# Optimization experiments

Hardware: AMD Instinct MI355X
Metric: run time of the kernel (lower is better)

Reference implementation:

```python
import jax, jax.numpy as jnp
import numpy as np

BIG = 1e9
EPS_BETA = 1e-6
EPS_BN = 1e-5

N_NODES = 50000
N_EDGES = 800000
IN_DIM = 128
OUT_DIM = 128


def setup_inputs() -> dict:
    key = jax.random.key(0)
    ks = jax.random.split(key, 8)
    h = jax.random.normal(ks[0], (N_NODES, IN_DIM), dtype=jnp.float32)
    src = jax.random.randint(ks[1], (N_EDGES,), 0, N_NODES, dtype=jnp.int32)
    dst = jax.random.randint(ks[2], (N_EDGES,), 0, N_NODES, dtype=jnp.int32)
    sigma_GD = jax.random.uniform(ks[3], (N_EDGES,), dtype=jnp.float32)
    fc_w = jax.random.normal(ks[4], (IN_DIM, OUT_DIM), dtype=jnp.float32) / np.sqrt(IN_DIM)
    fc_b = jax.random.normal(ks[5], (OUT_DIM,), dtype=jnp.float32) * 0.01
    attn_w = jax.random.normal(ks[6], (2 * OUT_DIM, 1), dtype=jnp.float32) / np.sqrt(2 * OUT_DIM)
    attn_b = jax.random.normal(ks[7], (1,), dtype=jnp.float32) * 0.01
    bn_gamma = jnp.ones((OUT_DIM,), dtype=jnp.float32)
    bn_beta = jnp.zeros((OUT_DIM,), dtype=jnp.float32)
    return {"h": h, "src": src, "dst": dst, "sigma_GD": sigma_GD,
            "fc_w": fc_w, "fc_b": fc_b, "attn_w": attn_w, "attn_b": attn_b,
            "bn_gamma": bn_gamma, "bn_beta": bn_beta}


def reference(h, src, dst, sigma_GD, fc_w, fc_b, attn_w, attn_b, bn_gamma, bn_beta):
    n = h.shape[0]
    # node projection
    z = h @ fc_w + fc_b                                   # [N, D]
    z = jnp.where(jnp.isinf(z), BIG, z)
    # per-edge attention logits: concat(src,dst) @ W == src@W1 + dst@W2 (avoid concat materialization)
    d = z.shape[1]
    w_src, w_dst = attn_w[:d], attn_w[d:]
    z_src = z[src]                                        # [E, D]
    a = z_src @ w_src + z[dst] @ w_dst + attn_b           # [E, 1]
    a = jnp.where(jnp.isinf(a), BIG, a)
    e = jax.nn.leaky_relu(a, negative_slope=0.01)[:, 0]   # [E]
    # segment softmax over incoming edges (mailbox softmax)
    m = jax.ops.segment_max(e, dst, num_segments=n)       # [N]
    ex = jnp.exp(e - m[dst])
    denom = jax.ops.segment_sum(ex, dst, num_segments=n)  # [N]
    alpha = ex / denom[dst]                               # [E]
    # beta: sigma_GD normalized per destination node
    bsum = jax.ops.segment_sum(sigma_GD, dst, num_segments=n)
    beta = sigma_GD / (bsum[dst] + EPS_BETA)              # [E]
    # weighted scatter-sum of source features
    h_new = jax.ops.segment_sum((alpha * beta)[:, None] * z_src, dst, num_segments=n)  # [N, D]
    h_new = jnp.where(jnp.isinf(h_new), BIG, h_new)
    # BatchNorm1d (training-mode batch stats, biased variance, as torch does)
    mu = h_new.mean(axis=0)
    var = ((h_new - mu) ** 2).mean(axis=0)
    h_bn = (h_new - mu) * jax.lax.rsqrt(var + EPS_BN) * bn_gamma + bn_beta
    return jax.nn.elu(h_bn)
```

## Files before the change

kernel.cpp:

```cpp
#include <hip/hip_runtime.h>
#include <hip/hip_fp16.h>
#include <math.h>

#define N_NODES 50000
#define N_EDGES 800000
#define BIGV 1000000000.0f
#define NBLK_SCAN 196
#define NBLK_GEMM 3125

typedef _Float16 half8 __attribute__((ext_vector_type(8)));
typedef float floatx4 __attribute__((ext_vector_type(4)));

__device__ __forceinline__ float clampinf(float x) { return isinf(x) ? BIGV : x; }

__global__ __launch_bounds__(256) void k_wcast(const float* __restrict__ W,
                                               __half* __restrict__ wt,
                                               int* __restrict__ cursor,
                                               float* __restrict__ bns)
{
    int idx = blockIdx.x * 256 + threadIdx.x;
    int n = idx >> 7, k = idx & 127;
    wt[idx] = __float2half(W[k * 128 + n]);
    for (int i = idx; i < N_NODES; i += 16384) cursor[i] = 0;
    if (idx < 256) bns[idx] = 0.f;
}

__global__ __launch_bounds__(256) void k_gemm(
    const float* __restrict__ h, const __half* __restrict__ wt,
    const float* __restrict__ bias, const float* __restrict__ attn_w,
    const int* __restrict__ dst, __half* __restrict__ zh,
    float* __restrict__ sv, float* __restrict__ tv,
    int* __restrict__ cursor, int* __restrict__ rank)
{
    __shared__ _Float16 hA[16][136];
    __shared__ float spart[4][16], tpart[4][16];

    const int tid = threadIdx.x;
    const int lane = tid & 63;
    const int wv = tid >> 6;
    const int l16 = lane & 15;
    const int oct = lane >> 4;
    const int n0 = wv << 5;
    const int node0 = blockIdx.x << 4;

    const int e = blockIdx.x * 256 + tid;
    const int d = dst[e];
    {
        const float4* h4 = (const float4*)(h + (size_t)node0 * 128);
        for (int i = tid; i < 512; i += 256) {
            int r = i >> 5, c4 = i & 31;
            float4 v = h4[i];
            union { __half2 h2[2]; uint2 u; } pk;
            pk.h2[0] = __floats2half2_rn(v.x, v.y);
            pk.h2[1] = __floats2half2_rn(v.z, v.w);
            *(uint2*)&hA[r][c4 << 2] = pk.u;
        }
    }
    rank[e] = atomicAdd(&cursor[d], 1);

    half8 bfrag[4][2];
    #pragma unroll
    for (int kk = 0; kk < 4; ++kk)
        #pragma unroll
        for (int t = 0; t < 2; ++t)
            bfrag[kk][t] = *(const half8*)(wt + (size_t)(n0 + t * 16 + l16) * 128
                                              + kk * 32 + oct * 8);

    const float bv0 = bias[n0 + l16],         bv1 = bias[n0 + 16 + l16];
    const float ws0 = attn_w[n0 + l16],       ws1 = attn_w[n0 + 16 + l16];
    const float wd0 = attn_w[128 + n0 + l16], wd1 = attn_w[128 + n0 + 16 + l16];

    __syncthreads();

    floatx4 acc0 = {0.f, 0.f, 0.f, 0.f};
    floatx4 acc1 = {0.f, 0.f, 0.f, 0.f};
    #pragma unroll
    for (int kk = 0; kk < 4; ++kk) {
        half8 a = *(const half8*)&hA[l16][(kk << 5) + (oct << 3)];
        acc0 = __builtin_amdgcn_mfma_f32_16x16x32_f16(a, bfrag[kk][0], acc0, 0, 0, 0);
        acc1 = __builtin_amdgcn_mfma_f32_16x16x32_f16(a, bfrag[kk][1], acc1, 0, 0, 0);
    }

    float s_acc[4], t_acc[4];
    #pragma unroll
    for (int r = 0; r < 4; ++r) {
        float z0 = clampinf(acc0[r] + bv0);
        float z1 = clampinf(acc1[r] + bv1);
        const int row = (oct << 2) + r;
        zh[(size_t)(node0 + row) * 128 + n0 + l16]      = __float2half(z0);
        zh[(size_t)(node0 + row) * 128 + n0 + 16 + l16] = __float2half(z1);
        s_acc[r] = z0 * ws0 + z1 * ws1;
        t_acc[r] = z0 * wd0 + z1 * wd1;
    }
    #pragma unroll
    for (int r = 0; r < 4; ++r) {
        #pragma unroll
        for (int o = 1; o < 16; o <<= 1) {
            s_acc[r] += __shfl_xor(s_acc[r], o);
            t_acc[r] += __shfl_xor(t_acc[r], o);
        }
    }
    if (l16 == 0) {
        #pragma unroll
        for (int r = 0; r < 4; ++r) {
            spart[wv][(oct << 2) + r] = s_acc[r];
            tpart[wv][(oct << 2) + r] = t_acc[r];
        }
    }
    __syncthreads();
    if (tid < 16) {
        sv[node0 + tid] = spart[0][tid] + spart[1][tid] + spart[2][tid] + spart[3][tid];
        tv[node0 + tid] = tpart[0][tid] + tpart[1][tid] + tpart[2][tid] + tpart[3][tid];
    }
}

__global__ __launch_bounds__(256) void k_scan_bsum(const int* __restrict__ cursor,
                                                   int* __restrict__ bsum)
{
    __shared__ int s[256];
    const int t = threadIdx.x;
    const int idx = blockIdx.x * 256 + t;
    s[t] = (idx < N_NODES) ? cursor[idx] : 0;
    __syncthreads();
    for (int off = 128; off; off >>= 1) {
        if (t < off) s[t] += s[t + off];
        __syncthreads();
    }
    if (t == 0) bsum[blockIdx.x] = s[0];
}

__global__ __launch_bounds__(256) void k_scan_final(const int* __restrict__ bsum,
                                                    const int* __restrict__ cursor_in,
                                                    int* __restrict__ colptr)
{
    __shared__ int rs[256];
    __shared__ int s[256];
    const int t = threadIdx.x;

    int rv = (t < NBLK_SCAN) ? bsum[t] : 0;
    rs[t] = rv;
    __syncthreads();
    for (int off = 1; off < 256; off <<= 1) {
        int u = (t >= off) ? rs[t - off] : 0;
        __syncthreads();
        rs[t] += u;
        __syncthreads();
    }
    const int broot = (blockIdx.x > 0) ? rs[blockIdx.x - 1] : 0;
    if (blockIdx.x == 0 && t == 255) colptr[N_NODES] = rs[255];

    const int idx = blockIdx.x * 256 + t;
    int v = (idx < N_NODES) ? cursor_in[idx] : 0;
    s[t] = v;
    __syncthreads();
    for (int off = 1; off < 256; off <<= 1) {
        int u = (t >= off) ? s[t - off] : 0;
        __syncthreads();
        s[t] += u;
        __syncthreads();
    }
    if (idx < N_NODES) colptr[idx] = broot + s[t] - v;
}

__global__ void k_scatter(const int* __restrict__ src, const int* __restrict__ dst,
                          const float* __restrict__ sigma,
                          const int* __restrict__ rank, const int* __restrict__ colptr,
                          const float* __restrict__ sv, const float* __restrict__ tv,
                          const float* __restrict__ attn_b,
                          float4* __restrict__ recs)
{
    int e = blockIdx.x * 256 + threadIdx.x;
    if (e < N_EDGES) {
        int s = src[e];
        int d = dst[e];
        float a = sv[s] + tv[d] + attn_b[0];
        a = clampinf(a);
        float ev = a > 0.f ? a : 0.01f * a;
        int pos = colptr[d] + rank[e];
        float4 rec;
        rec.x = __int_as_float(s);
        rec.y = sigma[e];
        rec.z = ev;
        rec.w = 0.f;
        recs[pos] = rec;
    }
}

__global__ __launch_bounds__(256) void k_agg(
    const int* __restrict__ colptr, const float4* __restrict__ recs,
    const __half* __restrict__ zh, float* __restrict__ out)
{
    const int lane = threadIdx.x & 63;
    const int node = blockIdx.x * 4 + (threadIdx.x >> 6);
    if (node >= N_NODES) return;
    const int base = colptr[node];
    const int deg = colptr[node + 1] - base;

    const int grp = lane >> 4;
    const int l16 = lane & 15;
    float acc[8] = {0.f, 0.f, 0.f, 0.f, 0.f, 0.f, 0.f, 0.f};

    if (deg > 0) {
        if (deg <= 64) {
            int sidx = 0; float sig = 0.f, e = -INFINITY;
            if (lane < deg) {
                float4 r = recs[base + lane];
                sidx = __float_as_int(r.x); sig = r.y; e = r.z;
            }
            float m = e;
            for (int o = 32; o; o >>= 1) m = fmaxf(m, __shfl_xor(m, o));
            float p = (lane < deg) ? __expf(e - m) : 0.f;
            float dn = p, bs = sig;
            for (int o = 32; o; o >>= 1) {
                dn += __shfl_xor(dn, o);
                bs += __shfl_xor(bs, o);
            }
            const float coef = p * sig * (1.0f / dn) / (bs + 1e-6f);
            for (int c = 0; c < deg; c += 4) {
                const int j = c + grp;
                const int js = (j < deg) ? j : 0;
                float cf = __shfl(coef, js);
                int sj = __shfl(sidx, js);
                if (j < deg) {
                    uint4 raw = *(const uint4*)(zh + ((size_t)sj << 7) + (l16 << 3));
                    const __half2* hp = (const __half2*)&raw;
                    #pragma unroll
                    for (int k = 0; k < 4; ++k) {
                        float2 f = __half22float2(hp[k]);
                        acc[2*k]   = fmaf(cf, f.x, acc[2*k]);
                        acc[2*k+1] = fmaf(cf, f.y, acc[2*k+1]);
                    }
                }
            }
        } else {
            float m = -INFINITY;
            for (int i = lane; i < deg; i += 64) m = fmaxf(m, recs[base + i].z);
            for (int o = 32; o; o >>= 1) m = fmaxf(m, __shfl_xor(m, o));
            float dn = 0.f, bs = 0.f;
            for (int i = lane; i < deg; i += 64) {
                float4 r = recs[base + i];
                dn += __expf(r.z - m); bs += r.y;
            }
            for (int o = 32; o; o >>= 1) {
                dn += __shfl_xor(dn, o);
                bs += __shfl_xor(bs, o);
            }
            const float scale = (1.0f / dn) / (bs + 1e-6f);
            for (int c = 0; c < deg; c += 64) {
                int i = c + lane;
                int sidx = 0; float coef = 0.f;
                if (i < deg) {
                    float4 r = recs[base + i];
                    sidx = __float_as_int(r.x);
                    coef = __expf(r.z - m) * r.y * scale;
                }
                const int cnt = min(64, deg - c);
                for (int j = 0; j < cnt; j += 4) {
                    const int jj = j + grp;
                    const int js = (jj < cnt) ? jj : 0;
                    float cf = __shfl(coef, js);
                    int sj = __shfl(sidx, js);
                    if (jj < cnt) {
                        uint4 raw = *(const uint4*)(zh + ((size_t)sj << 7) + (l16 << 3));
                        const __half2* hp = (const __half2*)&raw;
                        #pragma unroll
                        for (int k = 0; k < 4; ++k) {
                            float2 f = __half22float2(hp[k]);
                            acc[2*k]   = fmaf(cf, f.x, acc[2*k]);
                            acc[2*k+1] = fmaf(cf, f.y, acc[2*k+1]);
                        }
                    }
                }
            }
        }
    }
    #pragma unroll
    for (int k = 0; k < 8; ++k) {
        acc[k] += __shfl_xor(acc[k], 16);
        acc[k] += __shfl_xor(acc[k], 32);
    }
    if (grp == 0) {
        float4 o0, o1;
        o0.x = clampinf(acc[0]); o0.y = clampinf(acc[1]);
        o0.z = clampinf(acc[2]); o0.w = clampinf(acc[3]);
        o1.x = clampinf(acc[4]); o1.y = clampinf(acc[5]);
        o1.z = clampinf(acc[6]); o1.w = clampinf(acc[7]);
        float4* op = (float4*)(out + (size_t)node * 128 + (l16 << 3));
        op[0] = o0; op[1] = o1;
    }
}

__global__ __launch_bounds__(256) void k_bnstats(const float* __restrict__ hnew,
                                                 float* __restrict__ sums)
{
    const int f = threadIdx.x & 127;
    const int half_ = threadIdx.x >> 7;
    float s = 0.f, q = 0.f;
    for (int node = blockIdx.x * 2 + half_; node < N_NODES; node += gridDim.x * 2) {
        float v = hnew[(size_t)node * 128 + f];
        s += v;
        q += v * v;
    }
    __shared__ float ls[256], lq[256];
    ls[threadIdx.x] = s; lq[threadIdx.x] = q;
    __syncthreads();
    if (half_ == 0) {
        s += ls[threadIdx.x + 128];
        q += lq[threadIdx.x + 128];
        atomicAdd(&sums[f], s);
        atomicAdd(&sums[128 + f], q);
    }
}

__global__ __launch_bounds__(256) void k_bnapply(float* __restrict__ io,
                                                 const float* __restrict__ sums,
                                                 const float* __restrict__ gamma,
                                                 const float* __restrict__ beta)
{
    const size_t idx = (size_t)blockIdx.x * 256 + threadIdx.x;
    const int f = (int)(idx & 127);
    const float invn = 1.0f / (float)N_NODES;
    float mu = sums[f] * invn;
    float var = fmaxf(sums[128 + f] * invn - mu * mu, 0.f);
    float rs = rsqrtf(var + 1e-5f);
    float x = io[idx];
    float y = (x - mu) * rs * gamma[f] + beta[f];
    io[idx] = y > 0.f ? y : expm1f(y);
}

extern "C" void kernel_launch(void* const* d_in, const int* in_sizes, int n_in,
                              void* d_out, int out_size, void* d_ws, size_t ws_size,
                              hipStream_t stream)
{
    const float* h      = (const float*)d_in[0];
    const int*   src    = (const int*)  d_in[1];
    const int*   dst    = (const int*)  d_in[2];
    const float* sigma  = (const float*)d_in[3];
    const float* fc_w   = (const float*)d_in[4];
    const float* fc_b   = (const float*)d_in[5];
    const float* attn_w = (const float*)d_in[6];
    const float* attn_b = (const float*)d_in[7];
    const float* gamma  = (const float*)d_in[8];
    const float* beta   = (const float*)d_in[9];
    float* out = (float*)d_out;

    float4* recs   = (float4*)d_ws;
    __half* zh     = (__half*)(recs + N_EDGES);
    float*  sv     = (float*)(zh + (size_t)N_NODES * 128);
    float*  tv     = sv + N_NODES;
    float*  bns    = tv + N_NODES;
    int*    colptr = (int*)(bns + 256);
    int*    cursor = colptr + 50004;
    int*    bsum   = cursor + N_NODES;
    int*    broot  = bsum + 256;
    __half* wt     = (__half*)(broot + 256);
    int*    rank   = (int*)(wt + 128 * 128);

    k_wcast     <<<64, 256, 0, stream>>>(fc_w, wt, cursor, bns);
    k_gemm      <<<NBLK_GEMM, 256, 0, stream>>>(h, wt, fc_b, attn_w, dst,
                                                zh, sv, tv, cursor, rank);
    k_scan_bsum <<<NBLK_SCAN, 256, 0, stream>>>(cursor, bsum);
    k_scan_final<<<NBLK_SCAN, 256, 0, stream>>>(bsum, cursor, colptr);
    k_scatter   <<<N_EDGES / 256, 256, 0, stream>>>(src, dst, sigma, rank, colptr,
                                                    sv, tv, attn_b, recs);
    k_agg       <<<N_NODES / 4, 256, 0, stream>>>(colptr, recs, zh, out);
    k_bnstats   <<<256, 256, 0, stream>>>(out, bns);
    k_bnapply   <<<(N_NODES * 128) / 256, 256, 0, stream>>>(out, bns, gamma, beta);
}
```

Before: 230.8 us.

## Fuse all pipeline stages into one cooperative persistent kernel with grid syncs

Replaces the seven separate kernel launches (GEMM, two scan passes, scatter, aggregation, BN stats, BN apply) with a single cooperative persistent kernel that loops over work and uses grid-wide syncs between stages. The aim is to remove per-launch overhead and inter-kernel gaps. The BN apply step is also vectorised to float4. In exchange, the grid is capped by occupancy, so each stage gets fewer blocks, and each grid.sync adds its own cost; shared memory is reused through a union.

Result: slower. 883.2 us (+282.8%).

```diff
diff --git a/kernel.cpp b/kernel.cpp
--- a/kernel.cpp
+++ b/kernel.cpp
@@ -1,22 +1,31 @@
 #include <hip/hip_runtime.h>
+#include <hip/hip_cooperative_groups.h>
 #include <hip/hip_fp16.h>
 #include <math.h>
+
+namespace cg = cooperative_groups;
 
 #define N_NODES 50000
 #define N_EDGES 800000
 #define BIGV 1000000000.0f
 #define NBLK_SCAN 196
-#define NBLK_GEMM 3125
+#define N_TILES 3125
 
 typedef _Float16 half8 __attribute__((ext_vector_type(8)));
 typedef float floatx4 __attribute__((ext_vector_type(4)));
 
 __device__ __forceinline__ float clampinf(float x) { return isinf(x) ? BIGV : x; }
 
-__global__ __launch_bounds__(256) void k_wcast(const float* __restrict__ W,
-                                               __half* __restrict__ wt,
-                                               int* __restrict__ cursor,
-                                               float* __restrict__ bns)
+union SH {
+    struct { _Float16 hA[16][136]; float spart[4][16]; float tpart[4][16]; } g;
+    struct { int rs[256]; int s[256]; } sc;
+    struct { float ls[256]; float lq[256]; } bn;
+};
+
+__global__ __launch_bounds__(256) void k_pre(const float* __restrict__ W,
+                                             __half* __restrict__ wt,
+                                             int* __restrict__ cursor,
+                                             float* __restrict__ bns)
 {
     int idx = blockIdx.x * 256 + threadIdx.x;
     int n = idx >> 7, k = idx & 127;
@@ -25,152 +34,148 @@
     if (idx < 256) bns[idx] = 0.f;
 }
 
-__global__ __launch_bounds__(256) void k_gemm(
+__global__ __launch_bounds__(256) void k_mega(
     const float* __restrict__ h, const __half* __restrict__ wt,
     const float* __restrict__ bias, const float* __restrict__ attn_w,
-    const int* __restrict__ dst, __half* __restrict__ zh,
-    float* __restrict__ sv, float* __restrict__ tv,
-    int* __restrict__ cursor, int* __restrict__ rank)
+    const int* __restrict__ src, const int* __restrict__ dst,
+    const float* __restrict__ sigma, const float* __restrict__ attn_b,
+    __half* __restrict__ zh, float* __restrict__ sv, float* __restrict__ tv,
+    int* __restrict__ cursor, int* __restrict__ rank,
+    int* __restrict__ bsum, int* __restrict__ colptr,
+    float4* __restrict__ recs, float* __restrict__ out,
+    float* __restrict__ bns, const float* __restrict__ gamma,
+    const float* __restrict__ beta)
 {
-    __shared__ _Float16 hA[16][136];
-    __shared__ float spart[4][16], tpart[4][16];
+    __shared__ SH sh;
+    cg::grid_group grid = cg::this_grid();
 
     const int tid = threadIdx.x;
     const int lane = tid & 63;
     const int wv = tid >> 6;
     const int l16 = lane & 15;
     const int oct = lane >> 4;
-    const int n0 = wv << 5;
-    const int node0 = blockIdx.x << 4;
-
-    const int e = blockIdx.x * 256 + tid;
-    const int d = dst[e];
+
     {
-        const float4* h4 = (const float4*)(h + (size_t)node0 * 128);
-        for (int i = tid; i < 512; i += 256) {
-            int r = i >> 5, c4 = i & 31;
-            float4 v = h4[i];
-            union { __half2 h2[2]; uint2 u; } pk;
-            pk.h2[0] = __floats2half2_rn(v.x, v.y);
-            pk.h2[1] = __floats2half2_rn(v.z, v.w);
-            *(uint2*)&hA[r][c4 << 2] = pk.u;
-        }
-    }
-    rank[e] = atomicAdd(&cursor[d], 1);
-
-    half8 bfrag[4][2];
-    #pragma unroll
-    for (int kk = 0; kk < 4; ++kk)
+        const int n0 = wv << 5;
+        half8 bfrag[4][2];
         #pragma unroll
-        for (int t = 0; t < 2; ++t)
-            bfrag[kk][t] = *(const half8*)(wt + (size_t)(n0 + t * 16 + l16) * 128
-                                              + kk * 32 + oct * 8);
-
-    const float bv0 = bias[n0 + l16],         bv1 = bias[n0 + 16 + l16];
-    const float ws0 = attn_w[n0 + l16],       ws1 = attn_w[n0 + 16 + l16];
-    const float wd0 = attn_w[128 + n0 + l16], wd1 = attn_w[128 + n0 + 16 + l16];
-
-    __syncthreads();
-
-    floatx4 acc0 = {0.f, 0.f, 0.f, 0.f};
-    floatx4 acc1 = {0.f, 0.f, 0.f, 0.f};
-    #pragma unroll
-    for (int kk = 0; kk < 4; ++kk) {
-        half8 a = *(const half8*)&hA[l16][(kk << 5) + (oct << 3)];
-        acc0 = __builtin_amdgcn_mfma_f32_16x16x32_f16(a, bfrag[kk][0], acc0, 0, 0, 0);
-        acc1 = __builtin_amdgcn_mfma_f32_16x16x32_f16(a, bfrag[kk][1], acc1, 0, 0, 0);
-    }
-
-    float s_acc[4], t_acc[4];
-    #pragma unroll
-    for (int r = 0; r < 4; ++r) {
-        float z0 = clampinf(acc0[r] + bv0);
-        float z1 = clampinf(acc1[r] + bv1);
-        const int row = (oct << 2) + r;
-        zh[(size_t)(node0 + row) * 128 + n0 + l16]      = __float2half(z0);
-        zh[(size_t)(node0 + row) * 128 + n0 + 16 + l16] = __float2half(z1);
-        s_acc[r] = z0 * ws0 + z1 * ws1;
-        t_acc[r] = z0 * wd0 + z1 * wd1;
-    }
-    #pragma unroll
-    for (int r = 0; r < 4; ++r) {
-        #pragma unroll
-        for (int o = 1; o < 16; o <<= 1) {
-            s_acc[r] += __shfl_xor(s_acc[r], o);
-            t_acc[r] += __shfl_xor(t_acc[r], o);
-        }
-    }
-    if (l16 == 0) {
-        #pragma unroll
-        for (int r = 0; r < 4; ++r) {
-            spart[wv][(oct << 2) + r] = s_acc[r];
-            tpart[wv][(oct << 2) + r] = t_acc[r];
-        }
-    }
-    __syncthreads();
-    if (tid < 16) {
-        sv[node0 + tid] = spart[0][tid] + spart[1][tid] + spart[2][tid] + spart[3][tid];
-        tv[node0 + tid] = tpart[0][tid] + tpart[1][tid] + tpart[2][tid] + tpart[3][tid];
-    }
-}
-
-__global__ __launch_bounds__(256) void k_scan_bsum(const int* __restrict__ cursor,
-                                                   int* __restrict__ bsum)
-{
-    __shared__ int s[256];
-    const int t = threadIdx.x;
-    const int idx = blockIdx.x * 256 + t;
-    s[t] = (idx < N_NODES) ? cursor[idx] : 0;
-    __syncthreads();
-    for (int off = 128; off; off >>= 1) {
-        if (t < off) s[t] += s[t + off];
+        for (int kk = 0; kk < 4; ++kk)
+            #pragma unroll
+            for (int t = 0; t < 2; ++t)
+                bfrag[kk][t] = *(const half8*)(wt + (size_t)(n0 + t * 16 + l16) * 128
+                                                  + kk * 32 + oct * 8);
+        const float bv0 = bias[n0 + l16],         bv1 = bias[n0 + 16 + l16];
+        const float ws0 = attn_w[n0 + l16],       ws1 = attn_w[n0 + 16 + l16];
+        const float wd0 = attn_w[128 + n0 + l16], wd1 = attn_w[128 + n0 + 16 + l16];
+
+        for (int tile = blockIdx.x; tile < N_TILES; tile += gridDim.x) {
+            const int node0 = tile << 4;
+            const int e = tile * 256 + tid;
+            const int d = dst[e];
+            __syncthreads();
+            {
+                const float4* h4 = (const float4*)(h + (size_t)node0 * 128);
+                for (int i = tid; i < 512; i += 256) {
+                    int r = i >> 5, c4 = i & 31;
+                    float4 v = h4[i];
+                    union { __half2 h2[2]; uint2 u; } pk;
+                    pk.h2[0] = __floats2half2_rn(v.x, v.y);
+                    pk.h2[1] = __floats2half2_rn(v.z, v.w);
+                    *(uint2*)&sh.g.hA[r][c4 << 2] = pk.u;
+                }
+            }
+            rank[e] = atomicAdd(&cursor[d], 1);
+            __syncthreads();
+
+            floatx4 acc0 = {0.f, 0.f, 0.f, 0.f};
+            floatx4 acc1 = {0.f, 0.f, 0.f, 0.f};
+            #pragma unroll
+            for (int kk = 0; kk < 4; ++kk) {
+                half8 a = *(const half8*)&sh.g.hA[l16][(kk << 5) + (oct << 3)];
+                acc0 = __builtin_amdgcn_mfma_f32_16x16x32_f16(a, bfrag[kk][0], acc0, 0, 0, 0);
+                acc1 = __builtin_amdgcn_mfma_f32_16x16x32_f16(a, bfrag[kk][1], acc1, 0, 0, 0);
+            }
+
+            float s_acc[4], t_acc[4];
+            #pragma unroll
+            for (int r = 0; r < 4; ++r) {
+                float z0 = clampinf(acc0[r] + bv0);
+                float z1 = clampinf(acc1[r] + bv1);
+                const int row = (oct << 2) + r;
+                zh[(size_t)(node0 + row) * 128 + n0 + l16]      = __float2half(z0);
+                zh[(size_t)(node0 + row) * 128 + n0 + 16 + l16] = __float2half(z1);
+                s_acc[r] = z0 * ws0 + z1 * ws1;
+                t_acc[r] = z0 * wd0 + z1 * wd1;
+            }
+            #pragma unroll
+            for (int r = 0; r < 4; ++r) {
+                #pragma unroll
+                for (int o = 1; o < 16; o <<= 1) {
+                    s_acc[r] += __shfl_xor(s_acc[r], o);
+                    t_acc[r] += __shfl_xor(t_acc[r], o);
+                }
+            }
+            if (l16 == 0) {
+                #pragma unroll
+                for (int r = 0; r < 4; ++r) {
+                    sh.g.spart[wv][(oct << 2) + r] = s_acc[r];
+                    sh.g.tpart[wv][(oct << 2) + r] = t_acc[r];
+                }
+            }
+            __syncthreads();
+            if (tid < 16) {
+                sv[node0 + tid] = sh.g.spart[0][tid] + sh.g.spart[1][tid]
+                                + sh.g.spart[2][tid] + sh.g.spart[3][tid];
+                tv[node0 + tid] = sh.g.tpart[0][tid] + sh.g.tpart[1][tid]
+                                + sh.g.tpart[2][tid] + sh.g.tpart[3][tid];
+            }
+        }
+    }
+    __threadfence();
+    grid.sync();
+
+    if (blockIdx.x < NBLK_SCAN) {
+        const int idx = blockIdx.x * 256 + tid;
+        sh.sc.s[tid] = (idx < N_NODES) ? cursor[idx] : 0;
         __syncthreads();
-    }
-    if (t == 0) bsum[blockIdx.x] = s[0];
-}
-
-__global__ __launch_bounds__(256) void k_scan_final(const int* __restrict__ bsum,
-                                                    const int* __restrict__ cursor_in,
-                                                    int* __restrict__ colptr)
-{
-    __shared__ int rs[256];
-    __shared__ int s[256];
-    const int t = threadIdx.x;
-
-    int rv = (t < NBLK_SCAN) ? bsum[t] : 0;
-    rs[t] = rv;
-    __syncthreads();
-    for (int off = 1; off < 256; off <<= 1) {
-        int u = (t >= off) ? rs[t - off] : 0;
+        for (int off = 128; off; off >>= 1) {
+            if (tid < off) sh.sc.s[tid] += sh.sc.s[tid + off];
+            __syncthreads();
+        }
+        if (tid == 0) bsum[blockIdx.x] = sh.sc.s[0];
+    }
+    __threadfence();
+    grid.sync();
+
+    if (blockIdx.x < NBLK_SCAN) {
+        int rv = (tid < NBLK_SCAN) ? bsum[tid] : 0;
+        sh.sc.rs[tid] = rv;
         __syncthreads();
-        rs[t] += u;
+        for (int off = 1; off < 256; off <<= 1) {
+            int u = (tid >= off) ? sh.sc.rs[tid - off] : 0;
+            __syncthreads();
+            sh.sc.rs[tid] += u;
+            __syncthreads();
+        }
+        const int broot = (blockIdx.x > 0) ? sh.sc.rs[blockIdx.x - 1] : 0;
+        if (blockIdx.x == 0 && tid == 255) colptr[N_NODES] = sh.sc.rs[255];
+
+        const int idx = blockIdx.x * 256 + tid;
+        int v = (idx < N_NODES) ? cursor[idx] : 0;
+        sh.sc.s[tid] = v;
         __syncthreads();
-    }
-    const int broot = (blockIdx.x > 0) ? rs[blockIdx.x - 1] : 0;
-    if (blockIdx.x == 0 && t == 255) colptr[N_NODES] = rs[255];
-
-    const int idx = blockIdx.x * 256 + t;
-    int v = (idx < N_NODES) ? cursor_in[idx] : 0;
-    s[t] = v;
-    __syncthreads();
-    for (int off = 1; off < 256; off <<= 1) {
-        int u = (t >= off) ? s[t - off] : 0;
-        __syncthreads();
-        s[t] += u;
-        __syncthreads();
-    }
-    if (idx < N_NODES) colptr[idx] = broot + s[t] - v;
-}
-
-__global__ void k_scatter(const int* __restrict__ src, const int* __restrict__ dst,
-                          const float* __restrict__ sigma,
-                          const int* __restrict__ rank, const int* __restrict__ colptr,
-                          const float* __restrict__ sv, const float* __restrict__ tv,
-                          const float* __restrict__ attn_b,
-                          float4* __restrict__ recs)
-{
-    int e = blockIdx.x * 256 + threadIdx.x;
-    if (e < N_EDGES) {
+        for (int off = 1; off < 256; off <<= 1) {
+            int u = (tid >= off) ? sh.sc.s[tid - off] : 0;
+            __syncthreads();
+            sh.sc.s[tid] += u;
+            __syncthreads();
+        }
+        if (idx < N_NODES) colptr[idx] = broot + sh.sc.s[tid] - v;
+    }
+    __threadfence();
+    grid.sync();
+
+    for (int e = blockIdx.x * 256 + tid; e < N_EDGES; e += gridDim.x * 256) {
         int s = src[e];
         int d = dst[e];
         float a = sv[s] + tv[d] + attn_b[0];
@@ -184,83 +189,38 @@
         rec.w = 0.f;
         recs[pos] = rec;
     }
-}
-
-__global__ __launch_bounds__(256) void k_agg(
-    const int* __restrict__ colptr, const float4* __restrict__ recs,
-    const __half* __restrict__ zh, float* __restrict__ out)
-{
-    const int lane = threadIdx.x & 63;
-    const int node = blockIdx.x * 4 + (threadIdx.x >> 6);
-    if (node >= N_NODES) return;
-    const int base = colptr[node];
-    const int deg = colptr[node + 1] - base;
-
-    const int grp = lane >> 4;
-    const int l16 = lane & 15;
-    float acc[8] = {0.f, 0.f, 0.f, 0.f, 0.f, 0.f, 0.f, 0.f};
-
-    if (deg > 0) {
-        if (deg <= 64) {
-            int sidx = 0; float sig = 0.f, e = -INFINITY;
-            if (lane < deg) {
-                float4 r = recs[base + lane];
-                sidx = __float_as_int(r.x); sig = r.y; e = r.z;
-            }
-            float m = e;
-            for (int o = 32; o; o >>= 1) m = fmaxf(m, __shfl_xor(m, o));
-            float p = (lane < deg) ? __expf(e - m) : 0.f;
-            float dn = p, bs = sig;
-            for (int o = 32; o; o >>= 1) {
-                dn += __shfl_xor(dn, o);
-                bs += __shfl_xor(bs, o);
-            }
-            const float coef = p * sig * (1.0f / dn) / (bs + 1e-6f);
-            for (int c = 0; c < deg; c += 4) {
-                const int j = c + grp;
-                const int js = (j < deg) ? j : 0;
-                float cf = __shfl(coef, js);
-                int sj = __shfl(sidx, js);
-                if (j < deg) {
-                    uint4 raw = *(const uint4*)(zh + ((size_t)sj << 7) + (l16 << 3));
-                    const __half2* hp = (const __half2*)&raw;
-                    #pragma unroll
-                    for (int k = 0; k < 4; ++k) {
-                        float2 f = __half22float2(hp[k]);
-                        acc[2*k]   = fmaf(cf, f.x, acc[2*k]);
-                        acc[2*k+1] = fmaf(cf, f.y, acc[2*k+1]);
-                    }
-                }
-            }
-        } else {
-            float m = -INFINITY;
-            for (int i = lane; i < deg; i += 64) m = fmaxf(m, recs[base + i].z);
-            for (int o = 32; o; o >>= 1) m = fmaxf(m, __shfl_xor(m, o));
-            float dn = 0.f, bs = 0.f;
-            for (int i = lane; i < deg; i += 64) {
-                float4 r = recs[base + i];
-                dn += __expf(r.z - m); bs += r.y;
-            }
-            for (int o = 32; o; o >>= 1) {
-                dn += __shfl_xor(dn, o);
-                bs += __shfl_xor(bs, o);
-            }
-            const float scale = (1.0f / dn) / (bs + 1e-6f);
-            for (int c = 0; c < deg; c += 64) {
-                int i = c + lane;
-                int sidx = 0; float coef = 0.f;
-                if (i < deg) {
-                    float4 r = recs[base + i];
-                    sidx = __float_as_int(r.x);
-                    coef = __expf(r.z - m) * r.y * scale;
-                }
-                const int cnt = min(64, deg - c);
-                for (int j = 0; j < cnt; j += 4) {
-                    const int jj = j + grp;
-                    const int js = (jj < cnt) ? jj : 0;
+    __threadfence();
+    grid.sync();
+
+    for (int g4 = blockIdx.x; g4 < N_NODES / 4; g4 += gridDim.x) {
+        const int node = g4 * 4 + wv;
+        const int base = colptr[node];
+        const int deg = colptr[node + 1] - base;
+        const int grp = oct;
+        float acc[8] = {0.f, 0.f, 0.f, 0.f, 0.f, 0.f, 0.f, 0.f};
+
+        if (deg > 0) {
+            if (deg <= 64) {
+                int sidx = 0; float sig = 0.f, e = -INFINITY;
+                if (lane < deg) {
+                    float4 r = recs[base + lane];
+                    sidx = __float_as_int(r.x); sig = r.y; e = r.z;
+                }
+                float m = e;
+                for (int o = 32; o; o >>= 1) m = fmaxf(m, __shfl_xor(m, o));
+                float p = (lane < deg) ? __expf(e - m) : 0.f;
+                float dn = p, bs = sig;
+                for (int o = 32; o; o >>= 1) {
+                    dn += __shfl_xor(dn, o);
+                    bs += __shfl_xor(bs, o);
+                }
+                const float coef = p * sig * (1.0f / dn) / (bs + 1e-6f);
+                for (int c = 0; c < deg; c += 4) {
+                    const int j = c + grp;
+                    const int js = (j < deg) ? j : 0;
                     float cf = __shfl(coef, js);
                     int sj = __shfl(sidx, js);
-                    if (jj < cnt) {
+                    if (j < deg) {
                         uint4 raw = *(const uint4*)(zh + ((size_t)sj << 7) + (l16 << 3));
                         const __half2* hp = (const __half2*)&raw;
                         #pragma unroll
@@ -271,61 +231,126 @@
                         }
                     }
                 }
-            }
-        }
-    }
-    #pragma unroll
-    for (int k = 0; k < 8; ++k) {
-        acc[k] += __shfl_xor(acc[k], 16);
-        acc[k] += __shfl_xor(acc[k], 32);
-    }
-    if (grp == 0) {
-        float4 o0, o1;
-        o0.x = clampinf(acc[0]); o0.y = clampinf(acc[1]);
-        o0.z = clampinf(acc[2]); o0.w = clampinf(acc[3]);
-        o1.x = clampinf(acc[4]); o1.y = clampinf(acc[5]);
-        o1.z = clampinf(acc[6]); o1.w = clampinf(acc[7]);
-        float4* op = (float4*)(out + (size_t)node * 128 + (l16 << 3));
-        op[0] = o0; op[1] = o1;
-    }
-}
-
-__global__ __launch_bounds__(256) void k_bnstats(const float* __restrict__ hnew,
-                                                 float* __restrict__ sums)
-{
-    const int f = threadIdx.x & 127;
-    const int half_ = threadIdx.x >> 7;
-    float s = 0.f, q = 0.f;
-    for (int node = blockIdx.x * 2 + half_; node < N_NODES; node += gridDim.x * 2) {
-        float v = hnew[(size_t)node * 128 + f];
-        s += v;
-        q += v * v;
-    }
-    __shared__ float ls[256], lq[256];
-    ls[threadIdx.x] = s; lq[threadIdx.x] = q;
-    __syncthreads();
-    if (half_ == 0) {
-        s += ls[threadIdx.x + 128];
-        q += lq[threadIdx.x + 128];
-        atomicAdd(&sums[f], s);
-        atomicAdd(&sums[128 + f], q);
-    }
-}
-
-__global__ __launch_bounds__(256) void k_bnapply(float* __restrict__ io,
-                                                 const float* __restrict__ sums,
-                                                 const float* __restrict__ gamma,
-                                                 const float* __restrict__ beta)
-{
-    const size_t idx = (size_t)blockIdx.x * 256 + threadIdx.x;
-    const int f = (int)(idx & 127);
-    const float invn = 1.0f / (float)N_NODES;
-    float mu = sums[f] * invn;
-    float var = fmaxf(sums[128 + f] * invn - mu * mu, 0.f);
-    float rs = rsqrtf(var + 1e-5f);
-    float x = io[idx];
-    float y = (x - mu) * rs * gamma[f] + beta[f];
-    io[idx] = y > 0.f ? y : expm1f(y);
+            } else {
+                float m = -INFINITY;
+                for (int i = lane; i < deg; i += 64) m = fmaxf(m, recs[base + i].z);
+                for (int o = 32; o; o >>= 1) m = fmaxf(m, __shfl_xor(m, o));
+                float dn = 0.f, bs = 0.f;
+                for (int i = lane; i < deg; i += 64) {
+                    float4 r = recs[base + i];
+                    dn += __expf(r.z - m); bs += r.y;
+                }
+                for (int o = 32; o; o >>= 1) {
+                    dn += __shfl_xor(dn, o);
+                    bs += __shfl_xor(bs, o);
+                }
+                const float scale = (1.0f / dn) / (bs + 1e-6f);
+                for (int c = 0; c < deg; c += 64) {
+                    int i = c + lane;
+                    int sidx = 0; float coef = 0.f;
+                    if (i < deg) {
+                        float4 r = recs[base + i];
+                        sidx = __float_as_int(r.x);
+                        coef = __expf(r.z - m) * r.y * scale;
+                    }
+                    const int cnt = min(64, deg - c);
+                    for (int j = 0; j < cnt; j += 4) {
+                        const int jj = j + grp;
+                        const int js = (jj < cnt) ? jj : 0;
+                        float cf = __shfl(coef, js);
+                        int sj = __shfl(sidx, js);
+                        if (jj < cnt) {
+                            uint4 raw = *(const uint4*)(zh + ((size_t)sj << 7) + (l16 << 3));
+                            const __half2* hp = (const __half2*)&raw;
+                            #pragma unroll
+                            for (int k = 0; k < 4; ++k) {
+                                float2 f = __half22float2(hp[k]);
+                                acc[2*k]   = fmaf(cf, f.x, acc[2*k]);
+                                acc[2*k+1] = fmaf(cf, f.y, acc[2*k+1]);
+                            }
+                        }
+                    }
+                }
+            }
+        }
+        #pragma unroll
+        for (int k = 0; k < 8; ++k) {
+            acc[k] += __shfl_xor(acc[k], 16);
+            acc[k] += __shfl_xor(acc[k], 32);
+        }
+        if (grp == 0) {
+            float4 o0, o1;
+            o0.x = clampinf(acc[0]); o0.y = clampinf(acc[1]);
+            o0.z = clampinf(acc[2]); o0.w = clampinf(acc[3]);
+            o1.x = clampinf(acc[4]); o1.y = clampinf(acc[5]);
+            o1.z = clampinf(acc[6]); o1.w = clampinf(acc[7]);
+            float4* op = (float4*)(out + (size_t)node * 128 + (l16 << 3));
+            op[0] = o0; op[1] = o1;
+        }
+    }
+    __threadfence();
+    grid.sync();
+
+    {
+        const int f = tid & 127;
+        const int half_ = tid >> 7;
+        float s = 0.f, q = 0.f;
+        for (int node = blockIdx.x * 2 + half_; node < N_NODES; node += gridDim.x * 2) {
+            float v = out[(size_t)node * 128 + f];
+            s += v;
+            q += v * v;
+        }
+        sh.bn.ls[tid] = s; sh.bn.lq[tid] = q;
+        __syncthreads();
+        if (half_ == 0) {
+            s += sh.bn.ls[tid + 128];
+            q += sh.bn.lq[tid + 128];
+            atomicAdd(&bns[f], s);
+            atomicAdd(&bns[128 + f], q);
+        }
+    }
+    __threadfence();
+    grid.sync();
+
+    {
+        const float invn = 1.0f / (float)N_NODES;
+        const float4* s4 = (const float4*)bns;
+        const float4* q4 = (const float4*)(bns + 128);
+        const float4* g4p = (const float4*)gamma;
+        const float4* b4p = (const float4*)beta;
+        float4* io4 = (float4*)out;
+        const int total4 = (N_NODES * 128) / 4;
+        for (int i = blockIdx.x * 256 + tid; i < total4; i += gridDim.x * 256) {
+            const int f4 = i & 31;
+            float4 sm = s4[f4], sq = q4[f4], gm = g4p[f4], bt = b4p[f4];
+            float4 x = io4[i], y;
+            {
+                float mu = sm.x * invn, var = fmaxf(sq.x * invn - mu * mu, 0.f);
+                float r = rsqrtf(var + 1e-5f);
+                float t = (x.x - mu) * r * gm.x + bt.x;
+                y.x = t > 0.f ? t : expm1f(t);
+            }
+            {
+                float mu = sm.y * invn, var = fmaxf(sq.y * invn - mu * mu, 0.f);
+                float r = rsqrtf(var + 1e-5f);
+                float t = (x.y - mu) * r * gm.y + bt.y;
+                y.y = t > 0.f ? t : expm1f(t);
+            }
+            {
+                float mu = sm.z * invn, var = fmaxf(sq.z * invn - mu * mu, 0.f);
+                float r = rsqrtf(var + 1e-5f);
+                float t = (x.z - mu) * r * gm.z + bt.z;
+                y.z = t > 0.f ? t : expm1f(t);
+            }
+            {
+                float mu = sm.w * invn, var = fmaxf(sq.w * invn - mu * mu, 0.f);
+                float r = rsqrtf(var + 1e-5f);
+                float t = (x.w - mu) * r * gm.w + bt.w;
+                y.w = t > 0.f ? t : expm1f(t);
+            }
+            io4[i] = y;
+        }
+    }
 }
 
 extern "C" void kernel_launch(void* const* d_in, const int* in_sizes, int n_in,
@@ -356,14 +381,20 @@
     __half* wt     = (__half*)(broot + 256);
     int*    rank   = (int*)(wt + 128 * 128);
 
-    k_wcast     <<<64, 256, 0, stream>>>(fc_w, wt, cursor, bns);
-    k_gemm      <<<NBLK_GEMM, 256, 0, stream>>>(h, wt, fc_b, attn_w, dst,
-                                                zh, sv, tv, cursor, rank);
-    k_scan_bsum <<<NBLK_SCAN, 256, 0, stream>>>(cursor, bsum);
-    k_scan_final<<<NBLK_SCAN, 256, 0, stream>>>(bsum, cursor, colptr);
-    k_scatter   <<<N_EDGES / 256, 256, 0, stream>>>(src, dst, sigma, rank, colptr,
-                                                    sv, tv, attn_b, recs);
-    k_agg       <<<N_NODES / 4, 256, 0, stream>>>(colptr, recs, zh, out);
-    k_bnstats   <<<256, 256, 0, stream>>>(out, bns);
-    k_bnapply   <<<(N_NODES * 128) / 256, 256, 0, stream>>>(out, bns, gamma, beta);
+    int bpc = 0;
+    hipOccupancyMaxActiveBlocksPerMultiprocessor(&bpc, k_mega, 256, 0);
+    if (bpc < 1) bpc = 1;
+    long long grid_ll = (long long)bpc * 256;
+    if (grid_ll > N_TILES) grid_ll = N_TILES;
+    int grid = (int)grid_ll;
+    if (grid < 256) grid = 256;
+
+    k_pre<<<64, 256, 0, stream>>>(fc_w, wt, cursor, bns);
+
+    void* args[] = { (void*)&h, (void*)&wt, (void*)&fc_b, (void*)&attn_w,
+                     (void*)&src, (void*)&dst, (void*)&sigma, (void*)&attn_b,
+                     (void*)&zh, (void*)&sv, (void*)&tv, (void*)&cursor,
+                     (void*)&rank, (void*)&bsum, (void*)&colptr, (void*)&recs,
+                     (void*)&out, (void*)&bns, (void*)&gamma, (void*)&beta };
+    hipLaunchCooperativeKernel((void*)k_mega, dim3(grid), dim3(256), args, 0, stream);
 }
```
